# Optimization experiments

Measured on AMD Instinct MI355X. Metric: run time of the kernel, lower is better.

The kernel has to match this reference:

```python
import jax, jax.numpy as jnp
import numpy as np

N = 50000      # nodes
E = 500000     # edges
F_IN = 128     # num_features
H = 128        # hidden_dim
G = 256        # graphs in batch


def setup_inputs() -> dict:
    key = jax.random.key(0)
    ks = jax.random.split(key, 12)
    x = jax.random.normal(ks[0], (N, F_IN), jnp.float32)
    edge_index = jax.random.randint(ks[1], (2, E), 0, N, dtype=jnp.int32)
    edge_attr = jax.random.uniform(ks[2], (E,), jnp.float32)  # positive edge weights
    batch = jnp.sort(jax.random.randint(ks[3], (N,), 0, G, dtype=jnp.int32))
    s_in = 1.0 / np.sqrt(F_IN)
    s_h = 1.0 / np.sqrt(H)
    return {
        "x": x,
        "edge_index": edge_index,
        "edge_attr": edge_attr,
        "batch": batch,
        "W1": jax.random.normal(ks[4], (H, F_IN), jnp.float32) * s_in,
        "b1": jnp.zeros((H,), jnp.float32),
        "W2": jax.random.normal(ks[5], (H, H), jnp.float32) * s_h,
        "b2": jnp.zeros((H,), jnp.float32),
        "fW1": jax.random.normal(ks[6], (H, H), jnp.float32) * s_h,
        "fb1": jnp.zeros((H,), jnp.float32),
        "fW2": jax.random.normal(ks[7], (1, H), jnp.float32) * s_h,
        "fb2": jnp.zeros((1,), jnp.float32),
    }


def gcn_conv(x, src, dst, ew, W, b, n):
    """PyG GCNConv: linear transform, add self-loops (weight 1),
    symmetric deg^-1/2 normalization with edge weights, scatter-add, bias."""
    h = x @ W.T                                   # [n, H]
    loop = jnp.arange(n, dtype=src.dtype)
    s = jnp.concatenate([src, loop])
    d = jnp.concatenate([dst, loop])
    w = jnp.concatenate([ew, jnp.ones((n,), x.dtype)])
    deg = jax.ops.segment_sum(w, d, num_segments=n)  # weighted in-degree incl. self-loop
    dinv = jnp.where(deg > 0, jax.lax.rsqrt(deg), 0.0)
    norm = dinv[s] * w * dinv[d]                  # [E+n]
    msg = h[s] * norm[:, None]                    # gather + scale: [E+n, H]
    out = jax.ops.segment_sum(msg, d, num_segments=n)  # scatter-add
    return out + b


def reference(x, edge_index, edge_attr, batch, W1, b1, W2, b2, fW1, fb1, fW2, fb2):
    src, dst = edge_index[0], edge_index[1]
    h = jax.nn.relu(gcn_conv(x, src, dst, edge_attr, W1, b1, N))
    h = jax.nn.relu(gcn_conv(h, src, dst, edge_attr, W2, b2, N))
    # global_mean_pool over graph ids
    sums = jax.ops.segment_sum(h, batch, num_segments=G)            # [G, H]
    counts = jax.ops.segment_sum(jnp.ones((N,), h.dtype), batch, num_segments=G)
    pooled = sums / jnp.maximum(counts, 1.0)[:, None]
    o = jax.nn.relu(pooled @ fW1.T + fb1)
    return o @ fW2.T + fb2                                          # [G, 1]
```

## Files before the change

kernel.cpp:

```cpp
#include <hip/hip_runtime.h>
#include <hip/hip_bf16.h>


#define CAP 16
#define NREP 4
#define STRIDE 64

typedef __attribute__((ext_vector_type(8))) short short8;
typedef __attribute__((ext_vector_type(4))) float floatx4;

__device__ inline unsigned short f2bf(float f) {
    unsigned int u = __float_as_uint(f);
    u += 0x7FFF + ((u >> 16) & 1);
    return (unsigned short)(u >> 16);
}
__device__ inline float bf2f(unsigned short h) {
    return __uint_as_float(((unsigned int)h) << 16);
}

__global__ void build_csr(const int* __restrict__ src, const int* __restrict__ dst,
                          const float* __restrict__ ew,
                          int* __restrict__ cnt, int2* __restrict__ csr, int e, int n) {
    int i = blockIdx.x * blockDim.x + threadIdx.x;
    if (i < e) {
        int d = dst[i];
        int r = i & (NREP - 1);
        int pos = atomicAdd(&cnt[(size_t)r * n + d], 1);
        csr[((size_t)d << 6) + (r << 4) + pos] = make_int2(src[i], __float_as_int(ew[i]));
    }
}

__global__ __launch_bounds__(256) void deg_from_csr(const int* __restrict__ cnt,
        const int2* __restrict__ csr, float* __restrict__ dinv, int n) {
    int node = blockIdx.x * 8 + (threadIdx.x >> 5);
    int lane = threadIdx.x & 31;
    float s = 0.0f;
    if (node < n) {
        int pos = lane & 15;
        int sa = lane >> 4;
        int sb = 2 + (lane >> 4);
        int ca = cnt[(size_t)sa * n + node];
        int cb = cnt[(size_t)sb * n + node];
        const int2* b = csr + ((size_t)node << 6);
        if (pos < ca) s += __int_as_float(b[lane].y);
        if (pos < cb) s += __int_as_float(b[32 + lane].y);
    }
#pragma unroll
    for (int off = 16; off > 0; off >>= 1) s += __shfl_down(s, off, 32);
    if (node < n && lane == 0) dinv[node] = rsqrtf(s + 1.0f);
}

__global__ __launch_bounds__(256) void fold_compact(int* __restrict__ cnt,
        int2* __restrict__ csr, const float* __restrict__ dinv, int n) {
    int node = blockIdx.x * 8 + (threadIdx.x >> 5);
    if (node >= n) return;
    int lane = threadIdx.x & 31;
    int c0 = cnt[node];
    int c1 = cnt[(size_t)1 * n + node];
    int c2 = cnt[(size_t)2 * n + node];
    int c3 = cnt[(size_t)3 * n + node];
    int pre[4] = {0, c0, c0 + c1, c0 + c1 + c2};
    int cs[4] = {c0, c1, c2, c3};

    int2* b = csr + ((size_t)node << 6);
    int pos = lane & 15;
    int sa = lane >> 4;
    int sb = 2 + (lane >> 4);
    bool va = pos < cs[sa];
    bool vb = pos < cs[sb];
    int2 ea = va ? b[lane] : make_int2(0, 0);
    int2 eb = vb ? b[32 + lane] : make_int2(0, 0);
    if (va) ea.y = __float_as_int(__int_as_float(ea.y) * dinv[ea.x]);
    if (vb) eb.y = __float_as_int(__int_as_float(eb.y) * dinv[eb.x]);
    if (va) b[pre[sa] + pos] = ea;
    if (vb) b[pre[sb] + pos] = eb;
    if (lane == 0) cnt[node] = c0 + c1 + c2 + c3;
}

#define PW 136
__global__ __launch_bounds__(256) void gemm_f32_nt(const float* __restrict__ X,
        const float* __restrict__ W, unsigned short* __restrict__ C, int M) {
    __shared__ unsigned short whi[128 * PW];
    __shared__ unsigned short wlo[128 * PW];
    const int t = threadIdx.x;

    {
        int j = t >> 1;
        int c0 = (t & 1) * 64;
        const floatx4* wr = (const floatx4*)(W + (size_t)j * 128 + c0);
        unsigned short* dh = &whi[j * PW + c0];
        unsigned short* dl = &wlo[j * PW + c0];
#pragma unroll
        for (int i = 0; i < 16; ++i) {
            floatx4 v = wr[i];
            ushort4 hv, lv;
            hv.x = f2bf(v.x); lv.x = f2bf(v.x - bf2f(hv.x));
            hv.y = f2bf(v.y); lv.y = f2bf(v.y - bf2f(hv.y));
            hv.z = f2bf(v.z); lv.z = f2bf(v.z - bf2f(hv.z));
            hv.w = f2bf(v.w); lv.w = f2bf(v.w - bf2f(hv.w));
            *(ushort4*)(dh + i * 4) = hv;
            *(ushort4*)(dl + i * 4) = lv;
        }
    }
    __syncthreads();

    const int wave = t >> 6;
    const int lane = t & 63;
    const int q = lane >> 4;
    const int ln = lane & 15;
    const int rowbase = blockIdx.x * 128 + wave * 32;

    floatx4 acc[2][8];
#pragma unroll
    for (int s = 0; s < 2; ++s)
#pragma unroll
        for (int ct = 0; ct < 8; ++ct) acc[s][ct] = (floatx4){0.f, 0.f, 0.f, 0.f};

#pragma unroll
    for (int ks = 0; ks < 4; ++ks) {
        short8 ahi[2], alo[2];
#pragma unroll
        for (int s = 0; s < 2; ++s) {
            int row = rowbase + s * 16 + ln;
            int rowc = (row < M) ? row : (M - 1);
            const floatx4* xr = (const floatx4*)(X + (size_t)rowc * 128 + ks * 32 + q * 8);
            floatx4 x0 = xr[0];
            floatx4 x1 = xr[1];
            unsigned short h, l;
            h = f2bf(x0.x); l = f2bf(x0.x - bf2f(h)); ahi[s][0] = (short)h; alo[s][0] = (short)l;
            h = f2bf(x0.y); l = f2bf(x0.y - bf2f(h)); ahi[s][1] = (short)h; alo[s][1] = (short)l;
            h = f2bf(x0.z); l = f2bf(x0.z - bf2f(h)); ahi[s][2] = (short)h; alo[s][2] = (short)l;
            h = f2bf(x0.w); l = f2bf(x0.w - bf2f(h)); ahi[s][3] = (short)h; alo[s][3] = (short)l;
            h = f2bf(x1.x); l = f2bf(x1.x - bf2f(h)); ahi[s][4] = (short)h; alo[s][4] = (short)l;
            h = f2bf(x1.y); l = f2bf(x1.y - bf2f(h)); ahi[s][5] = (short)h; alo[s][5] = (short)l;
            h = f2bf(x1.z); l = f2bf(x1.z - bf2f(h)); ahi[s][6] = (short)h; alo[s][6] = (short)l;
            h = f2bf(x1.w); l = f2bf(x1.w - bf2f(h)); ahi[s][7] = (short)h; alo[s][7] = (short)l;
        }
#pragma unroll
        for (int ct = 0; ct < 8; ++ct) {
            int lidx = (ct * 16 + ln) * PW + ks * 32 + q * 8;
            short8 bhi = *(const short8*)&whi[lidx];
            short8 blo = *(const short8*)&wlo[lidx];
#pragma unroll
            for (int s = 0; s < 2; ++s) {
                acc[s][ct] = __builtin_amdgcn_mfma_f32_16x16x32_bf16(ahi[s], bhi, acc[s][ct], 0, 0, 0);
                acc[s][ct] = __builtin_amdgcn_mfma_f32_16x16x32_bf16(ahi[s], blo, acc[s][ct], 0, 0, 0);
                acc[s][ct] = __builtin_amdgcn_mfma_f32_16x16x32_bf16(alo[s], bhi, acc[s][ct], 0, 0, 0);
            }
        }
    }

#pragma unroll
    for (int s = 0; s < 2; ++s) {
#pragma unroll
        for (int r = 0; r < 4; ++r) {
            int row = rowbase + s * 16 + q * 4 + r;
            if (row < M) {
                unsigned short* cr = C + (size_t)row * 128 + ln;
#pragma unroll
                for (int ct = 0; ct < 8; ++ct) cr[ct * 16] = f2bf(acc[s][ct][r]);
            }
        }
    }
}

__global__ __launch_bounds__(256) void gemm_bf16_nt(const unsigned short* __restrict__ X,
        const float* __restrict__ W, unsigned short* __restrict__ C, int M) {
    __shared__ unsigned short whi[128 * PW];
    __shared__ unsigned short wlo[128 * PW];
    const int t = threadIdx.x;

    {
        int j = t >> 1;
        int c0 = (t & 1) * 64;
        const floatx4* wr = (const floatx4*)(W + (size_t)j * 128 + c0);
        unsigned short* dh = &whi[j * PW + c0];
        unsigned short* dl = &wlo[j * PW + c0];
#pragma unroll
        for (int i = 0; i < 16; ++i) {
            floatx4 v = wr[i];
            ushort4 hv, lv;
            hv.x = f2bf(v.x); lv.x = f2bf(v.x - bf2f(hv.x));
            hv.y = f2bf(v.y); lv.y = f2bf(v.y - bf2f(hv.y));
            hv.z = f2bf(v.z); lv.z = f2bf(v.z - bf2f(hv.z));
            hv.w = f2bf(v.w); lv.w = f2bf(v.w - bf2f(hv.w));
            *(ushort4*)(dh + i * 4) = hv;
            *(ushort4*)(dl + i * 4) = lv;
        }
    }
    __syncthreads();

    const int wave = t >> 6;
    const int lane = t & 63;
    const int q = lane >> 4;
    const int ln = lane & 15;
    const int rowbase = blockIdx.x * 128 + wave * 32;

    floatx4 acc[2][8];
#pragma unroll
    for (int s = 0; s < 2; ++s)
#pragma unroll
        for (int ct = 0; ct < 8; ++ct) acc[s][ct] = (floatx4){0.f, 0.f, 0.f, 0.f};

#pragma unroll
    for (int ks = 0; ks < 4; ++ks) {
        short8 a[2];
#pragma unroll
        for (int s = 0; s < 2; ++s) {
            int row = rowbase + s * 16 + ln;
            int rowc = (row < M) ? row : (M - 1);
            a[s] = *(const short8*)(X + (size_t)rowc * 128 + ks * 32 + q * 8);
        }
#pragma unroll
        for (int ct = 0; ct < 8; ++ct) {
            int lidx = (ct * 16 + ln) * PW + ks * 32 + q * 8;
            short8 bhi = *(const short8*)&whi[lidx];
            short8 blo = *(const short8*)&wlo[lidx];
#pragma unroll
            for (int s = 0; s < 2; ++s) {
                acc[s][ct] = __builtin_amdgcn_mfma_f32_16x16x32_bf16(a[s], bhi, acc[s][ct], 0, 0, 0);
                acc[s][ct] = __builtin_amdgcn_mfma_f32_16x16x32_bf16(a[s], blo, acc[s][ct], 0, 0, 0);
            }
        }
    }

#pragma unroll
    for (int s = 0; s < 2; ++s) {
#pragma unroll
        for (int r = 0; r < 4; ++r) {
            int row = rowbase + s * 16 + q * 4 + r;
            if (row < M) {
                unsigned short* cr = C + (size_t)row * 128 + ln;
#pragma unroll
                for (int ct = 0; ct < 8; ++ct) cr[ct * 16] = f2bf(acc[s][ct][r]);
            }
        }
    }
}

__global__ __launch_bounds__(256) void aggregate_finalize(
        const unsigned short* __restrict__ h, const unsigned short* __restrict__ hlin,
        const int* __restrict__ cnt, const int2* __restrict__ csr,
        const float* __restrict__ dinv, const float* __restrict__ bias,
        unsigned short* __restrict__ outb, int n) {
    int node = blockIdx.x * 8 + (threadIdx.x >> 5);
    if (node >= n) return;
    int lane = threadIdx.x & 31;
    float di = dinv[node];
    float sl = di * di;
    float4 b4 = ((const float4*)bias)[lane];
    ushort4 bse = ((const ushort4*)(hlin + (size_t)node * 128))[lane];
    float4 acc = make_float4(0.f, 0.f, 0.f, 0.f);

    const int2* b = csr + ((size_t)node << 6);
    const int4* bv = (const int4*)b;
    int c = cnt[node];
    int k = 0;
    for (; k + 4 <= c; k += 4) {
        int4 ea = bv[k >> 1];
        int4 eb = bv[(k >> 1) + 1];
        float w0 = __int_as_float(ea.y);
        float w1 = __int_as_float(ea.w);
        float w2 = __int_as_float(eb.y);
        float w3 = __int_as_float(eb.w);
        ushort4 h0 = ((const ushort4*)(h + (size_t)ea.x * 128))[lane];
        ushort4 h1 = ((const ushort4*)(h + (size_t)ea.z * 128))[lane];
        ushort4 h2 = ((const ushort4*)(h + (size_t)eb.x * 128))[lane];
        ushort4 h3 = ((const ushort4*)(h + (size_t)eb.z * 128))[lane];
        acc.x += bf2f(h0.x) * w0 + bf2f(h1.x) * w1 + bf2f(h2.x) * w2 + bf2f(h3.x) * w3;
        acc.y += bf2f(h0.y) * w0 + bf2f(h1.y) * w1 + bf2f(h2.y) * w2 + bf2f(h3.y) * w3;
        acc.z += bf2f(h0.z) * w0 + bf2f(h1.z) * w1 + bf2f(h2.z) * w2 + bf2f(h3.z) * w3;
        acc.w += bf2f(h0.w) * w0 + bf2f(h1.w) * w1 + bf2f(h2.w) * w2 + bf2f(h3.w) * w3;
    }
    if (k + 2 <= c) {
        int4 ea = bv[k >> 1];
        float w0 = __int_as_float(ea.y);
        float w1 = __int_as_float(ea.w);
        ushort4 h0 = ((const ushort4*)(h + (size_t)ea.x * 128))[lane];
        ushort4 h1 = ((const ushort4*)(h + (size_t)ea.z * 128))[lane];
        acc.x += bf2f(h0.x) * w0 + bf2f(h1.x) * w1;
        acc.y += bf2f(h0.y) * w0 + bf2f(h1.y) * w1;
        acc.z += bf2f(h0.z) * w0 + bf2f(h1.z) * w1;
        acc.w += bf2f(h0.w) * w0 + bf2f(h1.w) * w1;
        k += 2;
    }
    if (k < c) {
        int2 ed = b[k];
        float w = __int_as_float(ed.y);
        ushort4 hv = ((const ushort4*)(h + (size_t)ed.x * 128))[lane];
        acc.x += bf2f(hv.x) * w;
        acc.y += bf2f(hv.y) * w;
        acc.z += bf2f(hv.z) * w;
        acc.w += bf2f(hv.w) * w;
    }
    ushort4 o;
    o.x = f2bf(fmaxf(acc.x * di + bf2f(bse.x) * sl + b4.x, 0.0f));
    o.y = f2bf(fmaxf(acc.y * di + bf2f(bse.y) * sl + b4.y, 0.0f));
    o.z = f2bf(fmaxf(acc.z * di + bf2f(bse.z) * sl + b4.z, 0.0f));
    o.w = f2bf(fmaxf(acc.w * di + bf2f(bse.w) * sl + b4.w, 0.0f));
    ((ushort4*)(outb + (size_t)node * 128))[lane] = o;
}

#define POOL_BLOCKS 1024
__global__ __launch_bounds__(128) void pool_partial(const unsigned short* __restrict__ h,
        const int* __restrict__ batch, float* __restrict__ pooled, int n) {
    int chunk = (n + POOL_BLOCKS - 1) / POOL_BLOCKS;
    int s = blockIdx.x * chunk;
    if (s >= n) return;
    int e = min(s + chunk, n);
    int j = threadIdx.x;
    int curg = batch[s];
    float sum = 0.0f;
    for (int i = s; i < e; ++i) {
        int g = batch[i];
        if (g != curg) {
            atomicAdd(&pooled[(size_t)curg * 128 + j], sum);
            sum = 0.0f;
            curg = g;
        }
        sum += bf2f(h[(size_t)i * 128 + j]);
    }
    atomicAdd(&pooled[(size_t)curg * 128 + j], sum);
}

__global__ __launch_bounds__(128) void head_mlp(const float* __restrict__ pooled,
        const int* __restrict__ batch, int n,
        const float* __restrict__ fW1, const float* __restrict__ fb1,
        const float* __restrict__ fW2, const float* __restrict__ fb2,
        float* __restrict__ out) {
    int g = blockIdx.x;
    int j = threadIdx.x;
    int lo = 0, hi = n;
    while (lo < hi) { int mid = (lo + hi) >> 1; if (batch[mid] < g) lo = mid + 1; else hi = mid; }
    int s = lo;
    hi = n;
    while (lo < hi) { int mid = (lo + hi) >> 1; if (batch[mid] < g + 1) lo = mid + 1; else hi = mid; }
    int cnt = lo - s;
    float scale = 1.0f / fmaxf((float)cnt, 1.0f);

    __shared__ float row[128];
    __shared__ float part[2];
    row[j] = pooled[(size_t)g * 128 + j] * scale;
    __syncthreads();
    float acc = fb1[j];
    const float* wr = fW1 + (size_t)j * 128;
#pragma unroll 8
    for (int k = 0; k < 128; ++k) acc += row[k] * wr[k];
    float v = fmaxf(acc, 0.0f) * fW2[j];
#pragma unroll
    for (int off = 32; off > 0; off >>= 1) v += __shfl_down(v, off);
    if ((j & 63) == 0) part[j >> 6] = v;
    __syncthreads();
    if (j == 0) out[g] = part[0] + part[1] + fb2[0];
}

extern "C" void kernel_launch(void* const* d_in, const int* in_sizes, int n_in,
                              void* d_out, int out_size, void* d_ws, size_t ws_size,
                              hipStream_t stream) {
    const float* x   = (const float*)d_in[0];
    const int*   ei  = (const int*)d_in[1];
    const float* ew  = (const float*)d_in[2];
    const int* batch = (const int*)d_in[3];
    const float* W1  = (const float*)d_in[4];
    const float* b1  = (const float*)d_in[5];
    const float* W2  = (const float*)d_in[6];
    const float* b2  = (const float*)d_in[7];
    const float* fW1 = (const float*)d_in[8];
    const float* fb1 = (const float*)d_in[9];
    const float* fW2 = (const float*)d_in[10];
    const float* fb2 = (const float*)d_in[11];
    float* out = (float*)d_out;

    const int N = in_sizes[0] / 128;
    const int E = in_sizes[2];
    const int G = out_size;
    const int* src = ei;
    const int* dst = ei + E;

    unsigned short* A = (unsigned short*)d_ws;
    unsigned short* B = A + (size_t)N * 128;
    int2*  csr  = (int2*)(B + (size_t)N * 128);
    int*   cnt  = (int*)(csr + (size_t)N * STRIDE);
    float* dinv = (float*)(cnt + (size_t)NREP * N);
    float* pooled = dinv + N;

    hipMemsetAsync(cnt, 0, (size_t)NREP * N * sizeof(int), stream);
    build_csr<<<(E + 255) / 256, 256, 0, stream>>>(src, dst, ew, cnt, csr, E, N);
    deg_from_csr<<<(N + 7) / 8, 256, 0, stream>>>(cnt, csr, dinv, N);
    fold_compact<<<(N + 7) / 8, 256, 0, stream>>>(cnt, csr, dinv, N);

    gemm_f32_nt<<<(N + 127) / 128, 256, 0, stream>>>(x, W1, A, N);
    aggregate_finalize<<<(N + 7) / 8, 256, 0, stream>>>(A, A, cnt, csr, dinv, b1, B, N);

    gemm_bf16_nt<<<(N + 127) / 128, 256, 0, stream>>>(B, W2, A, N);
    aggregate_finalize<<<(N + 7) / 8, 256, 0, stream>>>(A, A, cnt, csr, dinv, b2, B, N);

    hipMemsetAsync(pooled, 0, (size_t)G * 128 * sizeof(float), stream);
    pool_partial<<<POOL_BLOCKS, 128, 0, stream>>>(B, batch, pooled, N);
    head_mlp<<<G, 128, 0, stream>>>(pooled, batch, N, fW1, fb1, fW2, fb2, out);
}
```

Baseline: 240.8 us.

## Split node features into four 32-column planes for cache-local aggregation

Hidden features are stored as four column-planes of 32 bf16 each, and aggregation launches four times as many blocks, one plane per block group. This shrinks each plane's gather working set so it fits better in cache. Each 32-lane group now handles four edges at once, with 8 lanes per edge, and reduces across lanes with shuffles. Edge lists are padded to a multiple of four with zero-weight entries. Degree computation is merged into the compaction kernel, followed by a separate dinv-folding pass. The cost is four reads of the CSR per layer and extra shuffle reductions.

```diff
diff --git a/kernel.cpp b/kernel.cpp
--- a/kernel.cpp
+++ b/kernel.cpp
@@ -30,28 +30,8 @@
     }
 }
 
-__global__ __launch_bounds__(256) void deg_from_csr(const int* __restrict__ cnt,
-        const int2* __restrict__ csr, float* __restrict__ dinv, int n) {
-    int node = blockIdx.x * 8 + (threadIdx.x >> 5);
-    int lane = threadIdx.x & 31;
-    float s = 0.0f;
-    if (node < n) {
-        int pos = lane & 15;
-        int sa = lane >> 4;
-        int sb = 2 + (lane >> 4);
-        int ca = cnt[(size_t)sa * n + node];
-        int cb = cnt[(size_t)sb * n + node];
-        const int2* b = csr + ((size_t)node << 6);
-        if (pos < ca) s += __int_as_float(b[lane].y);
-        if (pos < cb) s += __int_as_float(b[32 + lane].y);
-    }
-#pragma unroll
-    for (int off = 16; off > 0; off >>= 1) s += __shfl_down(s, off, 32);
-    if (node < n && lane == 0) dinv[node] = rsqrtf(s + 1.0f);
-}
-
-__global__ __launch_bounds__(256) void fold_compact(int* __restrict__ cnt,
-        int2* __restrict__ csr, const float* __restrict__ dinv, int n) {
+__global__ __launch_bounds__(256) void deg_compact(int* __restrict__ cnt,
+        int2* __restrict__ csr, float* __restrict__ dinv, int n) {
     int node = blockIdx.x * 8 + (threadIdx.x >> 5);
     if (node >= n) return;
     int lane = threadIdx.x & 31;
@@ -61,6 +41,8 @@
     int c3 = cnt[(size_t)3 * n + node];
     int pre[4] = {0, c0, c0 + c1, c0 + c1 + c2};
     int cs[4] = {c0, c1, c2, c3};
+    int ctot = c0 + c1 + c2 + c3;
+    int cp = (ctot + 3) & ~3;
 
     int2* b = csr + ((size_t)node << 6);
     int pos = lane & 15;
@@ -70,11 +52,35 @@
     bool vb = pos < cs[sb];
     int2 ea = va ? b[lane] : make_int2(0, 0);
     int2 eb = vb ? b[32 + lane] : make_int2(0, 0);
-    if (va) ea.y = __float_as_int(__int_as_float(ea.y) * dinv[ea.x]);
-    if (vb) eb.y = __float_as_int(__int_as_float(eb.y) * dinv[eb.x]);
+    float s = (va ? __int_as_float(ea.y) : 0.0f) + (vb ? __int_as_float(eb.y) : 0.0f);
+#pragma unroll
+    for (int off = 16; off > 0; off >>= 1) s += __shfl_down(s, off, 32);
     if (va) b[pre[sa] + pos] = ea;
     if (vb) b[pre[sb] + pos] = eb;
-    if (lane == 0) cnt[node] = c0 + c1 + c2 + c3;
+    if (lane < cp - ctot) b[ctot + lane] = make_int2(0, 0);
+    if (lane == 0) {
+        cnt[node] = cp;
+        dinv[node] = rsqrtf(s + 1.0f);
+    }
+}
+
+__global__ __launch_bounds__(256) void fold_dinv(const int* __restrict__ cnt,
+        int2* __restrict__ csr, const float* __restrict__ dinv, int n) {
+    int node = blockIdx.x * 8 + (threadIdx.x >> 5);
+    if (node >= n) return;
+    int lane = threadIdx.x & 31;
+    int cp = cnt[node];
+    int2* b = csr + ((size_t)node << 6);
+    if (lane < cp) {
+        int2 e = b[lane];
+        e.y = __float_as_int(__int_as_float(e.y) * dinv[e.x]);
+        b[lane] = e;
+    }
+    if (32 + lane < cp) {
+        int2 e = b[32 + lane];
+        e.y = __float_as_int(__int_as_float(e.y) * dinv[e.x]);
+        b[32 + lane] = e;
+    }
 }
 
 #define PW 136
@@ -83,6 +89,7 @@
     __shared__ unsigned short whi[128 * PW];
     __shared__ unsigned short wlo[128 * PW];
     const int t = threadIdx.x;
+    const size_t Np = (size_t)M * 32;
 
     {
         int j = t >> 1;
@@ -156,9 +163,10 @@
         for (int r = 0; r < 4; ++r) {
             int row = rowbase + s * 16 + q * 4 + r;
             if (row < M) {
-                unsigned short* cr = C + (size_t)row * 128 + ln;
-#pragma unroll
-                for (int ct = 0; ct < 8; ++ct) cr[ct * 16] = f2bf(acc[s][ct][r]);
+#pragma unroll
+                for (int ct = 0; ct < 8; ++ct)
+                    C[(size_t)(ct >> 1) * Np + (size_t)row * 32 + (ct & 1) * 16 + ln] =
+                        f2bf(acc[s][ct][r]);
             }
         }
     }
@@ -169,6 +177,7 @@
     __shared__ unsigned short whi[128 * PW];
     __shared__ unsigned short wlo[128 * PW];
     const int t = threadIdx.x;
+    const size_t Np = (size_t)M * 32;
 
     {
         int j = t >> 1;
@@ -209,7 +218,7 @@
         for (int s = 0; s < 2; ++s) {
             int row = rowbase + s * 16 + ln;
             int rowc = (row < M) ? row : (M - 1);
-            a[s] = *(const short8*)(X + (size_t)rowc * 128 + ks * 32 + q * 8);
+            a[s] = *(const short8*)(X + (size_t)ks * Np + (size_t)rowc * 32 + q * 8);
         }
 #pragma unroll
         for (int ct = 0; ct < 8; ++ct) {
@@ -230,9 +239,10 @@
         for (int r = 0; r < 4; ++r) {
             int row = rowbase + s * 16 + q * 4 + r;
             if (row < M) {
-                unsigned short* cr = C + (size_t)row * 128 + ln;
-#pragma unroll
-                for (int ct = 0; ct < 8; ++ct) cr[ct * 16] = f2bf(acc[s][ct][r]);
+#pragma unroll
+                for (int ct = 0; ct < 8; ++ct)
+                    C[(size_t)(ct >> 1) * Np + (size_t)row * 32 + (ct & 1) * 16 + ln] =
+                        f2bf(acc[s][ct][r]);
             }
         }
     }
@@ -242,63 +252,45 @@
         const unsigned short* __restrict__ h, const unsigned short* __restrict__ hlin,
         const int* __restrict__ cnt, const int2* __restrict__ csr,
         const float* __restrict__ dinv, const float* __restrict__ bias,
-        unsigned short* __restrict__ outb, int n) {
-    int node = blockIdx.x * 8 + (threadIdx.x >> 5);
+        unsigned short* __restrict__ outb, int n, int nb) {
+    int p = blockIdx.x / nb;
+    int node = (blockIdx.x % nb) * 8 + (threadIdx.x >> 5);
     if (node >= n) return;
     int lane = threadIdx.x & 31;
-    float di = dinv[node];
-    float sl = di * di;
-    float4 b4 = ((const float4*)bias)[lane];
-    ushort4 bse = ((const ushort4*)(hlin + (size_t)node * 128))[lane];
+    int esub = lane >> 3;
+    int fl = lane & 7;
+    const size_t Np = (size_t)n * 32;
+    const unsigned short* hp = h + (size_t)p * Np;
+
     float4 acc = make_float4(0.f, 0.f, 0.f, 0.f);
-
     const int2* b = csr + ((size_t)node << 6);
-    const int4* bv = (const int4*)b;
     int c = cnt[node];
-    int k = 0;
-    for (; k + 4 <= c; k += 4) {
-        int4 ea = bv[k >> 1];
-        int4 eb = bv[(k >> 1) + 1];
-        float w0 = __int_as_float(ea.y);
-        float w1 = __int_as_float(ea.w);
-        float w2 = __int_as_float(eb.y);
-        float w3 = __int_as_float(eb.w);
-        ushort4 h0 = ((const ushort4*)(h + (size_t)ea.x * 128))[lane];
-        ushort4 h1 = ((const ushort4*)(h + (size_t)ea.z * 128))[lane];
-        ushort4 h2 = ((const ushort4*)(h + (size_t)eb.x * 128))[lane];
-        ushort4 h3 = ((const ushort4*)(h + (size_t)eb.z * 128))[lane];
-        acc.x += bf2f(h0.x) * w0 + bf2f(h1.x) * w1 + bf2f(h2.x) * w2 + bf2f(h3.x) * w3;
-        acc.y += bf2f(h0.y) * w0 + bf2f(h1.y) * w1 + bf2f(h2.y) * w2 + bf2f(h3.y) * w3;
-        acc.z += bf2f(h0.z) * w0 + bf2f(h1.z) * w1 + bf2f(h2.z) * w2 + bf2f(h3.z) * w3;
-        acc.w += bf2f(h0.w) * w0 + bf2f(h1.w) * w1 + bf2f(h2.w) * w2 + bf2f(h3.w) * w3;
-    }
-    if (k + 2 <= c) {
-        int4 ea = bv[k >> 1];
-        float w0 = __int_as_float(ea.y);
-        float w1 = __int_as_float(ea.w);
-        ushort4 h0 = ((const ushort4*)(h + (size_t)ea.x * 128))[lane];
-        ushort4 h1 = ((const ushort4*)(h + (size_t)ea.z * 128))[lane];
-        acc.x += bf2f(h0.x) * w0 + bf2f(h1.x) * w1;
-        acc.y += bf2f(h0.y) * w0 + bf2f(h1.y) * w1;
-        acc.z += bf2f(h0.z) * w0 + bf2f(h1.z) * w1;
-        acc.w += bf2f(h0.w) * w0 + bf2f(h1.w) * w1;
-        k += 2;
-    }
-    if (k < c) {
-        int2 ed = b[k];
-        float w = __int_as_float(ed.y);
-        ushort4 hv = ((const ushort4*)(h + (size_t)ed.x * 128))[lane];
+    for (int k = 0; k < c; k += 4) {
+        int2 e = b[k + esub];
+        float w = __int_as_float(e.y);
+        ushort4 hv = *(const ushort4*)(hp + (size_t)e.x * 32 + fl * 4);
         acc.x += bf2f(hv.x) * w;
         acc.y += bf2f(hv.y) * w;
         acc.z += bf2f(hv.z) * w;
         acc.w += bf2f(hv.w) * w;
     }
-    ushort4 o;
-    o.x = f2bf(fmaxf(acc.x * di + bf2f(bse.x) * sl + b4.x, 0.0f));
-    o.y = f2bf(fmaxf(acc.y * di + bf2f(bse.y) * sl + b4.y, 0.0f));
-    o.z = f2bf(fmaxf(acc.z * di + bf2f(bse.z) * sl + b4.z, 0.0f));
-    o.w = f2bf(fmaxf(acc.w * di + bf2f(bse.w) * sl + b4.w, 0.0f));
-    ((ushort4*)(outb + (size_t)node * 128))[lane] = o;
+    acc.x += __shfl_xor(acc.x, 8, 32);  acc.y += __shfl_xor(acc.y, 8, 32);
+    acc.z += __shfl_xor(acc.z, 8, 32);  acc.w += __shfl_xor(acc.w, 8, 32);
+    acc.x += __shfl_xor(acc.x, 16, 32); acc.y += __shfl_xor(acc.y, 16, 32);
+    acc.z += __shfl_xor(acc.z, 16, 32); acc.w += __shfl_xor(acc.w, 16, 32);
+
+    if (esub == 0) {
+        float di = dinv[node];
+        float sl = di * di;
+        ushort4 hs = *(const ushort4*)(hlin + (size_t)p * Np + (size_t)node * 32 + fl * 4);
+        float4 b4 = ((const float4*)(bias + p * 32))[fl];
+        ushort4 o;
+        o.x = f2bf(fmaxf(acc.x * di + bf2f(hs.x) * sl + b4.x, 0.0f));
+        o.y = f2bf(fmaxf(acc.y * di + bf2f(hs.y) * sl + b4.y, 0.0f));
+        o.z = f2bf(fmaxf(acc.z * di + bf2f(hs.z) * sl + b4.z, 0.0f));
+        o.w = f2bf(fmaxf(acc.w * di + bf2f(hs.w) * sl + b4.w, 0.0f));
+        *(ushort4*)(outb + (size_t)p * Np + (size_t)node * 32 + fl * 4) = o;
+    }
 }
 
 #define POOL_BLOCKS 1024
@@ -309,6 +301,8 @@
     if (s >= n) return;
     int e = min(s + chunk, n);
     int j = threadIdx.x;
+    const size_t Np = (size_t)n * 32;
+    const unsigned short* hp = h + (size_t)(j >> 5) * Np + (j & 31);
     int curg = batch[s];
     float sum = 0.0f;
     for (int i = s; i < e; ++i) {
@@ -318,7 +312,7 @@
             sum = 0.0f;
             curg = g;
         }
-        sum += bf2f(h[(size_t)i * 128 + j]);
+        sum += bf2f(hp[(size_t)i * 32]);
     }
     atomicAdd(&pooled[(size_t)curg * 128 + j], sum);
 }
@@ -384,16 +378,18 @@
     float* dinv = (float*)(cnt + (size_t)NREP * N);
     float* pooled = dinv + N;
 
+    const int NB = (N + 7) / 8;
+
     hipMemsetAsync(cnt, 0, (size_t)NREP * N * sizeof(int), stream);
     build_csr<<<(E + 255) / 256, 256, 0, stream>>>(src, dst, ew, cnt, csr, E, N);
-    deg_from_csr<<<(N + 7) / 8, 256, 0, stream>>>(cnt, csr, dinv, N);
-    fold_compact<<<(N + 7) / 8, 256, 0, stream>>>(cnt, csr, dinv, N);
+    deg_compact<<<NB, 256, 0, stream>>>(cnt, csr, dinv, N);
+    fold_dinv<<<NB, 256, 0, stream>>>(cnt, csr, dinv, N);
 
     gemm_f32_nt<<<(N + 127) / 128, 256, 0, stream>>>(x, W1, A, N);
-    aggregate_finalize<<<(N + 7) / 8, 256, 0, stream>>>(A, A, cnt, csr, dinv, b1, B, N);
+    aggregate_finalize<<<4 * NB, 256, 0, stream>>>(A, A, cnt, csr, dinv, b1, B, N, NB);
 
     gemm_bf16_nt<<<(N + 127) / 128, 256, 0, stream>>>(B, W2, A, N);
-    aggregate_finalize<<<(N + 7) / 8, 256, 0, stream>>>(A, A, cnt, csr, dinv, b2, B, N);
+    aggregate_finalize<<<4 * NB, 256, 0, stream>>>(A, A, cnt, csr, dinv, b2, B, N, NB);
 
     hipMemsetAsync(pooled, 0, (size_t)G * 128 * sizeof(float), stream);
     pool_partial<<<POOL_BLOCKS, 128, 0, stream>>>(B, batch, pooled, N);
```

Result: slower. 287.5 us (+19.4%).
